# Kernel tuning notes

Measured on AMD Instinct MI355X. Metric: run time of the kernel, lower is better.

Reference implementation:

```python
import jax, jax.numpy as jnp
import numpy as np

D_MODEL = 1024
NHEAD = 16
HEAD_DIM = D_MODEL // NHEAD
MASK_FILLER = -1e20


def setup_inputs() -> dict:
    key = jax.random.key(0)
    ks = jax.random.split(key, 8)
    B, S = 2, 2048
    query = jax.random.normal(ks[0], (B, S, D_MODEL), dtype=jnp.float32)
    key_t = jax.random.normal(ks[1], (B, S, D_MODEL), dtype=jnp.float32)
    value = jax.random.normal(ks[2], (B, S, D_MODEL), dtype=jnp.float32)
    mask = jax.random.randint(ks[3], (B, S, S), 0, 2, dtype=jnp.int32)
    # nn.Linear(d_model, d_model, bias=False) weights, shape [out, in]
    scale = 1.0 / np.sqrt(D_MODEL)
    wq = jax.random.uniform(ks[4], (D_MODEL, D_MODEL), jnp.float32, -scale, scale)
    wk = jax.random.uniform(ks[5], (D_MODEL, D_MODEL), jnp.float32, -scale, scale)
    wv = jax.random.uniform(ks[6], (D_MODEL, D_MODEL), jnp.float32, -scale, scale)
    wo = jax.random.uniform(ks[7], (D_MODEL, D_MODEL), jnp.float32, -scale, scale)
    return {"query": query, "key": key_t, "value": value, "mask": mask,
            "wq": wq, "wk": wk, "wv": wv, "wo": wo}


def reference(query, key, value, mask, wq, wk, wv, wo):
    B = query.shape[0]
    # Projections: nn.Linear -> x @ W.T
    q = (query @ wq.T).reshape(B, -1, NHEAD, HEAD_DIM).transpose(0, 2, 1, 3)  # [B,H,Sq,Dh]
    k = (key @ wk.T).reshape(B, -1, NHEAD, HEAD_DIM).transpose(0, 2, 1, 3)    # [B,H,Sk,Dh]
    v = (value @ wv.T).reshape(B, -1, NHEAD, HEAD_DIM).transpose(0, 2, 1, 3)  # [B,H,Sk,Dh]
    scores = jnp.einsum('bhqd,bhkd->bhqk', q, k) / jnp.sqrt(jnp.float32(HEAD_DIM))
    scores = jnp.where(mask[:, None, :, :] == 0, MASK_FILLER, scores)
    attn = jax.nn.softmax(scores, axis=-1)  # dropout p=0.0 -> identity
    out = jnp.einsum('bhqk,bhkd->bhqd', attn, v)  # [B,H,Sq,Dh]
    out = out.transpose(0, 2, 1, 3).reshape(B, -1, D_MODEL)
    return out @ wo.T
```

## Files before the change

kernel.cpp:

```cpp
#include <hip/hip_runtime.h>
#include <stdint.h>

typedef __bf16 bf16x8 __attribute__((ext_vector_type(8)));
typedef float floatx4 __attribute__((ext_vector_type(4)));
typedef unsigned short ushort8v __attribute__((ext_vector_type(8)));
typedef unsigned int uint4v __attribute__((ext_vector_type(4)));
typedef unsigned int uint2v __attribute__((ext_vector_type(2)));
typedef unsigned short u16;
typedef unsigned long long u64;

#define GLOAD_LDS16(gp, lp)                                                       \
  __builtin_amdgcn_global_load_lds((__attribute__((address_space(1))) void*)(gp), \
                                   (__attribute__((address_space(3))) void*)(lp), \
                                   16, 0, 0)

__device__ __forceinline__ u16 f2bf(float f) {
  uint32_t u = __builtin_bit_cast(uint32_t, f);
  u = (u + 0x7FFFu + ((u >> 16) & 1u)) >> 16;
  return (u16)u;
}

__device__ __forceinline__ ushort8v load8(const void* base, size_t elemOff, int isf32) {
  if (isf32) {
    const uint32_t* p = (const uint32_t*)base + elemOff;
    uint4v a = *(const uint4v*)p;
    uint4v b = *(const uint4v*)(p + 4);
#pragma unroll
    for (int i = 0; i < 4; ++i) { a[i] += 0x8000u; b[i] += 0x8000u; }
    uint4v r;
    r[0] = __builtin_amdgcn_perm(a[1], a[0], 0x07060302);
    r[1] = __builtin_amdgcn_perm(a[3], a[2], 0x07060302);
    r[2] = __builtin_amdgcn_perm(b[1], b[0], 0x07060302);
    r[3] = __builtin_amdgcn_perm(b[3], b[2], 0x07060302);
    return __builtin_bit_cast(ushort8v, r);
  }
  return *(const ushort8v*)((const u16*)base + elemOff);
}

__global__ void detect_dtype(const u16* __restrict__ q, int* __restrict__ flag) {
  if (threadIdx.x == 0) *flag = 0;
  __syncthreads();
  int hit = 0;
  for (int i = threadIdx.x; i < 8192; i += 256) {
    u16 u = q[i];
    if (((u >> 7) & 0xFF) == 0xFF) hit = 1;
  }
  if (hit) atomicOr(flag, 1);
}

__global__ __launch_bounds__(256)
void prep(const void* X0, const void* X1, const void* X2,
          const void* W0, const void* W1, const void* W2, const void* W3,
          u16* __restrict__ Xb, u16* __restrict__ Wb,
          const int* __restrict__ mask, u64* __restrict__ mpk,
          const int* __restrict__ flagp)
{
  const int id = blockIdx.x;
  const int t  = threadIdx.x;
  if (id < 8192) {
    const int isf = *flagp;
    const int r2  = t >> 7;
    const int col = (t & 127) * 8;
    const void* src; u16* dst; int row;
    if (id < 6144) {
      const int s = id >> 11;
      src = (s == 0) ? X0 : (s == 1) ? X1 : X2;
      row = (id & 2047) * 2 + r2;
      dst = Xb + (size_t)s * 4096 * 1040 + (size_t)row * 1040 + col;
    } else {
      const int s = (id - 6144) >> 9;
      src = (s == 0) ? W0 : (s == 1) ? W1 : (s == 2) ? W2 : W3;
      row = ((id - 6144) & 511) * 2 + r2;
      dst = Wb + (size_t)s * 1024 * 1040 + (size_t)row * 1040 + col;
    }
    *(ushort8v*)dst = load8(src, (size_t)row * 1024 + col, isf);
  } else {
    const int g    = (id - 8192) * 4 + (t >> 6);
    const int lane = t & 63;
#pragma unroll
    for (int i = 0; i < 4; ++i) {
      const int wordId = g * 4 + i;
      const int row  = wordId >> 5;
      const int word = wordId & 31;
      const int m = mask[(size_t)row * 2048 + word * 64 + lane];
      u64 bits = __ballot(m != 0);
      if (lane == 0) mpk[(size_t)row * 32 + word] = bits;
    }
  }
}

__global__ void pack_mask(const int* __restrict__ mask, u64* __restrict__ mpk) {
  const int gw   = (blockIdx.x * 256 + threadIdx.x) >> 6;
  const int lane = threadIdx.x & 63;
  const int word = gw & 31;
  const int row  = gw >> 5;
  const int m = mask[(size_t)row * 2048 + word * 64 + lane];
  u64 bits = __ballot(m != 0);
  if (lane == 0) mpk[(size_t)row * 32 + word] = bits;
}

__global__ __launch_bounds__(256)
void cvt_w(const void* W0, const void* W1, const void* W2, const void* W3,
           u16* __restrict__ dst, const int* __restrict__ flagp) {
  const int isf = *flagp;
  const int z = blockIdx.y;
  const void* src = (z == 0) ? W0 : (z == 1) ? W1 : (z == 2) ? W2 : W3;
  const size_t off = ((size_t)blockIdx.x * 256 + threadIdx.x) * 8;
  *(ushort8v*)(dst + (size_t)z * 1024 * 1024 + off) = load8(src, off, isf);
}

__global__ __launch_bounds__(256, 3)
void gemm_qkv_b(const u16* __restrict__ Xb, const u16* __restrict__ Wb,
                u16* __restrict__ Qb, u16* __restrict__ Kb, u16* __restrict__ Vt)
{
  const int AS = 1040, WS = 1040, N = 1024, K = 1024;
  const int z = blockIdx.z;
  const u16* A = Xb + (size_t)z * 4096 * AS;
  const u16* W = Wb + (size_t)z * 1024 * WS;

  __shared__ __align__(16) u16 lA[2 * 128 * 32];
  __shared__ __align__(16) u16 lB[2 * 128 * 32];

  const int tid  = threadIdx.x;
  const int lane = tid & 63;
  const int quad = lane >> 4;
  const int l15  = lane & 15;
  const int w    = tid >> 6;
  const int wm   = w >> 1, wn = w & 1;
  const int tileM = blockIdx.x * 128;
  const int tileN = blockIdx.y * 128;

  floatx4 acc[4][4] = {};

  const int ldRow = tid >> 2;
  const int ldCol = (tid & 3) * 8;
  const u16* aG = A + (size_t)(tileM + ldRow) * AS + ldCol;
  const u16* bG = W + (size_t)(tileN + ldRow) * WS + ldCol;
  u16* lAp = lA + tid * 8;
  u16* lBp = lB + tid * 8;

  GLOAD_LDS16(aG, lAp);
  GLOAD_LDS16(aG + (size_t)64 * AS, lAp + 2048);
  GLOAD_LDS16(bG, lBp);
  GLOAD_LDS16(bG + (size_t)64 * WS, lBp + 2048);
  __syncthreads();

#pragma unroll 2
  for (int k0 = 0; k0 < K; k0 += 32) {
    const int cur = (k0 >> 5) & 1;
    const int nxo = 4096 * (cur ^ 1);
    if (k0 + 32 < K) {
      GLOAD_LDS16(aG + k0 + 32, lAp + nxo);
      GLOAD_LDS16(aG + (size_t)64 * AS + k0 + 32, lAp + nxo + 2048);
      GLOAD_LDS16(bG + k0 + 32, lBp + nxo);
      GLOAD_LDS16(bG + (size_t)64 * WS + k0 + 32, lBp + nxo + 2048);
    }
    const u16* cA = lA + 4096 * cur;
    const u16* cB = lB + 4096 * cur;
    bf16x8 af[4], bw[4];
#pragma unroll
    for (int i = 0; i < 4; ++i) {
      af[i] = *(const bf16x8*)&cA[(wm * 64 + i * 16 + l15) * 32 + quad * 8];
      bw[i] = *(const bf16x8*)&cB[(wn * 64 + i * 16 + l15) * 32 + quad * 8];
    }
#pragma unroll
    for (int i = 0; i < 4; ++i)
#pragma unroll
      for (int j = 0; j < 4; ++j)
        acc[i][j] = __builtin_amdgcn_mfma_f32_16x16x32_bf16(af[i], bw[j], acc[i][j], 0, 0, 0);
    __syncthreads();
  }

  if (z < 2) {
    u16* C = (z == 0) ? Qb : Kb;
    const float sc = (z == 0) ? 0.18033688011112042f : 1.0f;
#pragma unroll
    for (int i = 0; i < 4; ++i) {
      const int row0 = tileM + wm * 64 + i * 16 + quad * 4;
#pragma unroll
      for (int j = 0; j < 4; ++j) {
        const int col = tileN + wn * 64 + j * 16 + l15;
#pragma unroll
        for (int r = 0; r < 4; ++r)
          C[(size_t)(row0 + r) * N + col] = f2bf(acc[i][j][r] * sc);
      }
    }
  } else {
    const int half = w >> 1;
    u16* myT = (w & 1) ? lB : lA;
#pragma unroll
    for (int pass = 0; pass < 2; ++pass) {
      __syncthreads();
      if (half == pass) {
#pragma unroll
        for (int i = 0; i < 4; ++i)
#pragma unroll
          for (int j = 0; j < 4; ++j)
#pragma unroll
            for (int r = 0; r < 4; ++r) {
              const int lr = i * 16 + quad * 4 + r;
              const int lc = j * 16 + l15;
              myT[lr * 64 + (lc ^ (quad << 4))] = f2bf(acc[i][j][r]);
            }
      }
      __syncthreads();
      if (half == pass) {
        const int n    = lane;
        const int gcol = tileN + wn * 64 + n;
        const int hh = gcol >> 6, dd = gcol & 63;
        const int growBase = tileM + wm * 64;
        const int bb = growBase >> 11;
        const int s0 = growBase & 2047;
        u16* dst = Vt + (((size_t)bb * 16 + hh) * 64 + dd) * 2048 + s0;
#pragma unroll
        for (int m0 = 0; m0 < 64; m0 += 8) {
          ushort8v pk;
#pragma unroll
          for (int t = 0; t < 8; ++t) {
            const int m = m0 + t;
            pk[t] = myT[m * 64 + (n ^ ((m & 12) << 2))];
          }
          *(ushort8v*)(dst + m0) = pk;
        }
      }
    }
  }
}

__global__ __launch_bounds__(256)
void gemm_qkv_f(const void* X0, const void* X1, const void* X2,
                const u16* __restrict__ Wb,
                u16* __restrict__ Qb, u16* __restrict__ Kb, u16* __restrict__ Vt,
                const int* __restrict__ flagp)
{
  const int K = 1024, N = 1024;
  const int isf = *flagp;
  const int z = blockIdx.z;
  const void* A_ = (z == 0) ? X0 : (z == 1) ? X1 : X2;
  const u16* W = Wb + (size_t)z * 1024 * 1024;

  __shared__ __align__(16) u16 lA[128 * 32];
  __shared__ __align__(16) u16 lB[128 * 32];

  const int tid  = threadIdx.x;
  const int lane = tid & 63;
  const int quad = lane >> 4;
  const int l15  = lane & 15;
  const int w    = tid >> 6;
  const int wm   = w >> 1, wn = w & 1;
  const int tileM = blockIdx.x * 128;
  const int tileN = blockIdx.y * 128;

  floatx4 acc[4][4] = {};

  const int ldRow = tid >> 2;
  const int ldCol = (tid & 3) * 8;
  const size_t aOff = (size_t)(tileM + ldRow) * K + ldCol;
  const u16* bG = W + (size_t)(tileN + ldRow) * K + ldCol;
  u16* lAp = lA + tid * 8;
  u16* lBp = lB + tid * 8;

  ushort8v a0 = load8(A_, aOff, isf);
  ushort8v a1 = load8(A_, aOff + (size_t)64 * K, isf);
  ushort8v b0 = *(const ushort8v*)bG;
  ushort8v b1 = *(const ushort8v*)(bG + (size_t)64 * K);

  for (int k0 = 0; k0 < K; k0 += 32) {
    __syncthreads();
    *(ushort8v*)lAp          = a0;
    *(ushort8v*)(lAp + 2048) = a1;
    *(ushort8v*)lBp          = b0;
    *(ushort8v*)(lBp + 2048) = b1;
    __syncthreads();

    if (k0 + 32 < K) {
      a0 = load8(A_, aOff + k0 + 32, isf);
      a1 = load8(A_, aOff + (size_t)64 * K + k0 + 32, isf);
      b0 = *(const ushort8v*)(bG + k0 + 32);
      b1 = *(const ushort8v*)(bG + (size_t)64 * K + k0 + 32);
    }

    bf16x8 af[4], bw[4];
#pragma unroll
    for (int i = 0; i < 4; ++i) {
      af[i] = *(const bf16x8*)&lA[(wm * 64 + i * 16 + l15) * 32 + quad * 8];
      bw[i] = *(const bf16x8*)&lB[(wn * 64 + i * 16 + l15) * 32 + quad * 8];
    }
#pragma unroll
    for (int i = 0; i < 4; ++i)
#pragma unroll
      for (int j = 0; j < 4; ++j)
        acc[i][j] = __builtin_amdgcn_mfma_f32_16x16x32_bf16(af[i], bw[j], acc[i][j], 0, 0, 0);
  }

  if (z < 2) {
    u16* C = (z == 0) ? Qb : Kb;
    const float sc = (z == 0) ? 0.18033688011112042f : 1.0f;
#pragma unroll
    for (int i = 0; i < 4; ++i) {
      const int row0 = tileM + wm * 64 + i * 16 + quad * 4;
#pragma unroll
      for (int j = 0; j < 4; ++j) {
        const int col = tileN + wn * 64 + j * 16 + l15;
#pragma unroll
        for (int r = 0; r < 4; ++r)
          C[(size_t)(row0 + r) * N + col] = f2bf(acc[i][j][r] * sc);
      }
    }
  } else {
    const int half = w >> 1;
    u16* myT = (w & 1) ? lB : lA;
#pragma unroll
    for (int pass = 0; pass < 2; ++pass) {
      __syncthreads();
      if (half == pass) {
#pragma unroll
        for (int i = 0; i < 4; ++i)
#pragma unroll
          for (int j = 0; j < 4; ++j)
#pragma unroll
            for (int r = 0; r < 4; ++r) {
              const int lr = i * 16 + quad * 4 + r;
              const int lc = j * 16 + l15;
              myT[lr * 64 + (lc ^ (quad << 4))] = f2bf(acc[i][j][r]);
            }
      }
      __syncthreads();
      if (half == pass) {
        const int n    = lane;
        const int gcol = tileN + wn * 64 + n;
        const int hh = gcol >> 6, dd = gcol & 63;
        const int growBase = tileM + wm * 64;
        const int bb = growBase >> 11;
        const int s0 = growBase & 2047;
        u16* dst = Vt + (((size_t)bb * 16 + hh) * 64 + dd) * 2048 + s0;
#pragma unroll
        for (int m0 = 0; m0 < 64; m0 += 8) {
          ushort8v pk;
#pragma unroll
          for (int t = 0; t < 8; ++t) {
            const int m = m0 + t;
            pk[t] = myT[m * 64 + (n ^ ((m & 12) << 2))];
          }
          *(ushort8v*)(dst + m0) = pk;
        }
      }
    }
  }
}

__global__ __launch_bounds__(256)
void attn(const u16* Qb, const u16* __restrict__ Kb, const u16* __restrict__ Vt,
          const u64* __restrict__ mpk, u16* AO, int aoStr)
{
  __shared__ __align__(16) u16 lK[2][64 * 64];
  __shared__ __align__(16) u16 lV[64 * 64];
  __shared__ __align__(16) u16 lP[4][16 * 64];

  const int tid  = threadIdx.x;
  const int lane = tid & 63;
  const int quad = lane >> 4;
  const int l15  = lane & 15;
  const int w    = tid >> 6;

  const int bh = blockIdx.x;
  const int qt = blockIdx.y;
  const int b  = bh >> 4;
  const int h  = bh & 15;
  const size_t rowB   = (size_t)b * 2048;
  const size_t vtBase = ((size_t)bh * 64) * 2048;

  bf16x8 aq[2];
  {
    const u16* qp = Qb + (rowB + qt * 64 + w * 16 + l15) * 1024 + h * 64 + quad * 8;
    aq[0] = *(const bf16x8*)qp;
    aq[1] = *(const bf16x8*)(qp + 32);
  }

  const ushort8v one_u = {0x3F80, 0x3F80, 0x3F80, 0x3F80, 0x3F80, 0x3F80, 0x3F80, 0x3F80};
  const bf16x8 ones = __builtin_bit_cast(bf16x8, one_u);

  floatx4 o[4], l4;
#pragma unroll
  for (int nb = 0; nb < 4; ++nb) o[nb] = (floatx4){0.f, 0.f, 0.f, 0.f};
  l4 = (floatx4){0.f, 0.f, 0.f, 0.f};

  const u64* mrow = mpk + (rowB + qt * 64 + w * 16 + l15) * 32;
  u16* lPw = &lP[w][0];

  const int r1 = tid >> 3;
  const int cs = ((tid & 7) ^ (r1 & 7)) * 8;
  const u16* kSrc = Kb + (rowB + r1) * 1024 + h * 64 + cs;
  const u16* vSrc = Vt + vtBase + (size_t)r1 * 2048 + cs;

  GLOAD_LDS16(kSrc,                     &lK[0][tid * 8]);
  GLOAD_LDS16(kSrc + (size_t)32 * 1024, &lK[0][tid * 8 + 2048]);

#pragma unroll 2
  for (int kt = 0; kt < 32; ++kt) {
    const int cur = kt & 1;
    __syncthreads();

    {
      const u16* vS = vSrc + kt * 64;
      GLOAD_LDS16(vS,                     &lV[tid * 8]);
      GLOAD_LDS16(vS + (size_t)32 * 2048, &lV[tid * 8 + 2048]);
    }
    if (kt < 31) {
      const u16* kS = kSrc + (size_t)(kt + 1) * 64 * 1024;
      GLOAD_LDS16(kS,                     &lK[cur ^ 1][tid * 8]);
      GLOAD_LDS16(kS + (size_t)32 * 1024, &lK[cur ^ 1][tid * 8 + 2048]);
    }

    const u64 mw = mrow[kt];

#pragma unroll
    for (int nb = 0; nb < 4; ++nb) {
      const int row = nb * 16 + l15;
      const int swk = (row & 7) << 3;
      bf16x8 ak0 = *(const bf16x8*)&lK[cur][row * 64 + ((quad * 8) ^ swk)];
      bf16x8 ak1 = *(const bf16x8*)&lK[cur][row * 64 + ((quad * 8 + 32) ^ swk)];
      floatx4 sacc = {0.f, 0.f, 0.f, 0.f};
      sacc = __builtin_amdgcn_mfma_f32_16x16x32_bf16(ak0, aq[0], sacc, 0, 0, 0);
      sacc = __builtin_amdgcn_mfma_f32_16x16x32_bf16(ak1, aq[1], sacc, 0, 0, 0);
      const uint32_t nib = (uint32_t)(mw >> (nb * 16 + quad * 4)) & 0xFu;
      float p0 = (nib & 1u) ? __builtin_amdgcn_exp2f(sacc[0]) : 0.0f;
      float p1 = (nib & 2u) ? __builtin_amdgcn_exp2f(sacc[1]) : 0.0f;
      float p2 = (nib & 4u) ? __builtin_amdgcn_exp2f(sacc[2]) : 0.0f;
      float p3 = (nib & 8u) ? __builtin_amdgcn_exp2f(sacc[3]) : 0.0f;
      const uint32_t b0 = __builtin_bit_cast(uint32_t, p0) + 0x8000u;
      const uint32_t b1 = __builtin_bit_cast(uint32_t, p1) + 0x8000u;
      const uint32_t b2 = __builtin_bit_cast(uint32_t, p2) + 0x8000u;
      const uint32_t b3 = __builtin_bit_cast(uint32_t, p3) + 0x8000u;
      uint2v pk2;
      pk2[0] = __builtin_amdgcn_perm(b1, b0, 0x07060302);
      pk2[1] = __builtin_amdgcn_perm(b3, b2, 0x07060302);
      const int col = (nb * 16 + quad * 4) ^ ((l15 & 7) << 3);
      *(uint2v*)&lPw[l15 * 64 + col] = pk2;
    }
    __syncthreads();

#pragma unroll
    for (int ks = 0; ks < 2; ++ks) {
      bf16x8 ap = *(const bf16x8*)&lPw[l15 * 64 + ((ks * 32 + quad * 8) ^ ((l15 & 7) << 3))];
#pragma unroll
      for (int nb = 0; nb < 4; ++nb) {
        const int row = nb * 16 + l15;
        bf16x8 bv = *(const bf16x8*)&lV[row * 64 + ((ks * 32 + quad * 8) ^ ((row & 7) << 3))];
        o[nb] = __builtin_amdgcn_mfma_f32_16x16x32_bf16(ap, bv, o[nb], 0, 0, 0);
      }
      l4 = __builtin_amdgcn_mfma_f32_16x16x32_bf16(ap, ones, l4, 0, 0, 0);
    }
  }

#pragma unroll
  for (int r = 0; r < 4; ++r) {
    const float inv = 1.0f / l4[r];
    const size_t orow = (rowB + qt * 64 + w * 16 + quad * 4 + r) * aoStr + h * 64;
#pragma unroll
    for (int nb = 0; nb < 4; ++nb)
      AO[orow + nb * 16 + l15] = f2bf(o[nb][r] * inv);
  }
}

__global__ __launch_bounds__(256, 3)
void gemm_out(const u16* __restrict__ A, int aStr,
              const u16* __restrict__ W, int wStr, void* C_,
              const int* __restrict__ flagp)
{
  const int K = 1024, N = 1024;
  const int isf = *flagp;

  __shared__ __align__(16) u16 lA[2 * 64 * 32];
  __shared__ __align__(16) u16 lB[2 * 128 * 32];

  const int tid  = threadIdx.x;
  const int lane = tid & 63;
  const int quad = lane >> 4;
  const int l15  = lane & 15;
  const int w    = tid >> 6;
  const int tileM = blockIdx.x * 64;
  const int tileN = blockIdx.y * 128;

  floatx4 acc[4][2] = {};

  const int ldRow = tid >> 2;
  const int ldCol = (tid & 3) * 8;
  const u16* aG = A + (size_t)(tileM + ldRow) * aStr + ldCol;
  const u16* bG = W + (size_t)(tileN + ldRow) * wStr + ldCol;
  u16* lAp = lA + tid * 8;
  u16* lBp = lB + tid * 8;

  GLOAD_LDS16(aG, lAp);
  GLOAD_LDS16(bG, lBp);
  GLOAD_LDS16(bG + (size_t)64 * wStr, lBp + 2048);
  __syncthreads();

#pragma unroll 2
  for (int k0 = 0; k0 < K; k0 += 32) {
    const int cur = (k0 >> 5) & 1;
    const int nxA = 2048 * (cur ^ 1);
    const int nxB = 4096 * (cur ^ 1);
    if (k0 + 32 < K) {
      GLOAD_LDS16(aG + k0 + 32, lAp + nxA);
      GLOAD_LDS16(bG + k0 + 32, lBp + nxB);
      GLOAD_LDS16(bG + (size_t)64 * wStr + k0 + 32, lBp + nxB + 2048);
    }
    const u16* cA = lA + 2048 * cur;
    const u16* cB = lB + 4096 * cur;
    bf16x8 af[4], bw[2];
#pragma unroll
    for (int i = 0; i < 4; ++i)
      af[i] = *(const bf16x8*)&cA[(i * 16 + l15) * 32 + quad * 8];
#pragma unroll
    for (int j = 0; j < 2; ++j)
      bw[j] = *(const bf16x8*)&cB[(w * 32 + j * 16 + l15) * 32 + quad * 8];
#pragma unroll
    for (int i = 0; i < 4; ++i)
#pragma unroll
      for (int j = 0; j < 2; ++j)
        acc[i][j] = __builtin_amdgcn_mfma_f32_16x16x32_bf16(af[i], bw[j], acc[i][j], 0, 0, 0);
    __syncthreads();
  }

#pragma unroll
  for (int i = 0; i < 4; ++i) {
    const int row0 = tileM + i * 16 + quad * 4;
#pragma unroll
    for (int j = 0; j < 2; ++j) {
      const int col = tileN + w * 32 + j * 16 + l15;
#pragma unroll
      for (int r = 0; r < 4; ++r) {
        const size_t off = (size_t)(row0 + r) * N + col;
        if (isf) ((float*)C_)[off] = acc[i][j][r];
        else     ((u16*)C_)[off]   = f2bf(acc[i][j][r]);
      }
    }
  }
}

extern "C" void kernel_launch(void* const* d_in, const int* in_sizes, int n_in,
                              void* d_out, int out_size, void* d_ws, size_t ws_size,
                              hipStream_t stream)
{
  const int* mk = (const int*)d_in[3];

  int* flag = (int*)d_ws;
  u64* mpk  = (u64*)((char*)d_ws + 256);
  const size_t SZ = (size_t)4096 * 1024;
  u16* Qb = (u16*)((char*)d_ws + 256 + (size_t)1048576);
  u16* Kb = Qb + SZ;
  u16* Vt = Kb + SZ;
  u16* Wb = Vt + SZ;

  const size_t WB_PAD = (size_t)4 * 1024 * 1040;
  const size_t XB_PAD = (size_t)3 * 4096 * 1040;
  const size_t NEED = 256 + 1048576 + 3 * SZ * 2 + WB_PAD * 2 + XB_PAD * 2;

  detect_dtype<<<1, 256, 0, stream>>>((const u16*)d_in[0], flag);

  if (ws_size >= NEED) {
    u16* Xb = Wb + WB_PAD;
    prep<<<16384, 256, 0, stream>>>(d_in[0], d_in[1], d_in[2],
                                    d_in[4], d_in[5], d_in[6], d_in[7],
                                    Xb, Wb, mk, mpk, flag);
    gemm_qkv_b<<<dim3(32, 8, 3), 256, 0, stream>>>(Xb, Wb, Qb, Kb, Vt);
    u16* AOp = Xb;
    attn<<<dim3(32, 32), 256, 0, stream>>>(Qb, Kb, Vt, mpk, AOp, 1040);
    gemm_out<<<dim3(64, 8), 256, 0, stream>>>(AOp, 1040,
                                              Wb + (size_t)3 * 1024 * 1040, 1040,
                                              d_out, flag);
  } else {
    pack_mask<<<32768, 256, 0, stream>>>(mk, mpk);
    cvt_w<<<dim3(512, 4), 256, 0, stream>>>(d_in[4], d_in[5], d_in[6], d_in[7], Wb, flag);
    gemm_qkv_f<<<dim3(32, 8, 3), 256, 0, stream>>>(d_in[0], d_in[1], d_in[2],
                                                   Wb, Qb, Kb, Vt, flag);
    attn<<<dim3(32, 32), 256, 0, stream>>>(Qb, Kb, Vt, mpk, Qb, 1024);
    gemm_out<<<dim3(64, 8), 256, 0, stream>>>(Qb, 1024,
                                              Wb + (size_t)3 * 1024 * 1024, 1024,
                                              d_out, flag);
  }
}
```

Baseline: 274.5 us.

## Software-pipeline attention loop: overlap QK of next tile with PV of previous

Restructures the attention inner loop into a software pipeline. QK^T and softmax for tile kt now run in the same iteration as the PV product for tile kt-1, with V and P double-buffered in LDS. This removes one barrier per iteration and lets MFMA work from both phases interleave with the exp2 work. In exchange it doubles LDS use for V and P, which may lower occupancy. It also switches the bf16 packing from a manual round-and-perm to compiler __bf16 conversions.

Result: slower. 305.3 us (+11.2%).

```diff
diff --git a/kernel.cpp b/kernel.cpp
--- a/kernel.cpp
+++ b/kernel.cpp
@@ -2,6 +2,7 @@
 #include <stdint.h>
 
 typedef __bf16 bf16x8 __attribute__((ext_vector_type(8)));
+typedef __bf16 bf16x4 __attribute__((ext_vector_type(4)));
 typedef float floatx4 __attribute__((ext_vector_type(4)));
 typedef unsigned short ushort8v __attribute__((ext_vector_type(8)));
 typedef unsigned int uint4v __attribute__((ext_vector_type(4)));
@@ -349,13 +350,64 @@
   }
 }
 
+#define MFMA_BF16 __builtin_amdgcn_mfma_f32_16x16x32_bf16
+
+#define QK_PHASE(KBUF, sacc)                                                    \
+  {                                                                             \
+    _Pragma("unroll")                                                           \
+    for (int nb = 0; nb < 4; ++nb) {                                            \
+      const int row = nb * 16 + l15;                                            \
+      const int swk = (row & 7) << 3;                                           \
+      bf16x8 ak0 = *(const bf16x8*)&(KBUF)[row * 64 + ((quad * 8) ^ swk)];      \
+      bf16x8 ak1 = *(const bf16x8*)&(KBUF)[row * 64 + ((quad * 8 + 32) ^ swk)]; \
+      floatx4 s = {0.f, 0.f, 0.f, 0.f};                                         \
+      s = MFMA_BF16(ak0, aq[0], s, 0, 0, 0);                                    \
+      s = MFMA_BF16(ak1, aq[1], s, 0, 0, 0);                                    \
+      sacc[nb] = s;                                                             \
+    }                                                                           \
+  }
+
+#define PV_PHASE(PBUF, VBUF)                                                    \
+  {                                                                             \
+    _Pragma("unroll")                                                           \
+    for (int ks = 0; ks < 2; ++ks) {                                            \
+      bf16x8 ap = *(const bf16x8*)&(PBUF)[l15 * 64 +                            \
+                    ((ks * 32 + quad * 8) ^ ((l15 & 7) << 3))];                 \
+      _Pragma("unroll")                                                         \
+      for (int nb = 0; nb < 4; ++nb) {                                          \
+        const int row = nb * 16 + l15;                                          \
+        bf16x8 bv = *(const bf16x8*)&(VBUF)[row * 64 +                          \
+                      ((ks * 32 + quad * 8) ^ ((row & 7) << 3))];               \
+        o[nb] = MFMA_BF16(ap, bv, o[nb], 0, 0, 0);                              \
+      }                                                                         \
+      l4 = MFMA_BF16(ap, ones, l4, 0, 0, 0);                                    \
+    }                                                                           \
+  }
+
+#define SM_PHASE(sacc, mw, PDST)                                                \
+  {                                                                             \
+    _Pragma("unroll")                                                           \
+    for (int nb = 0; nb < 4; ++nb) {                                            \
+      const uint32_t nib = (uint32_t)((mw) >> (nb * 16 + quad * 4)) & 0xFu;     \
+      const float p0 = (nib & 1u) ? __builtin_amdgcn_exp2f(sacc[nb][0]) : 0.0f; \
+      const float p1 = (nib & 2u) ? __builtin_amdgcn_exp2f(sacc[nb][1]) : 0.0f; \
+      const float p2 = (nib & 4u) ? __builtin_amdgcn_exp2f(sacc[nb][2]) : 0.0f; \
+      const float p3 = (nib & 8u) ? __builtin_amdgcn_exp2f(sacc[nb][3]) : 0.0f; \
+      bf16x4 pk4;                                                               \
+      pk4[0] = (__bf16)p0; pk4[1] = (__bf16)p1;                                 \
+      pk4[2] = (__bf16)p2; pk4[3] = (__bf16)p3;                                 \
+      const int col = (nb * 16 + quad * 4) ^ ((l15 & 7) << 3);                  \
+      *(bf16x4*)&(PDST)[l15 * 64 + col] = pk4;                                  \
+    }                                                                           \
+  }
+
 __global__ __launch_bounds__(256)
 void attn(const u16* Qb, const u16* __restrict__ Kb, const u16* __restrict__ Vt,
           const u64* __restrict__ mpk, u16* AO, int aoStr)
 {
   __shared__ __align__(16) u16 lK[2][64 * 64];
-  __shared__ __align__(16) u16 lV[64 * 64];
-  __shared__ __align__(16) u16 lP[4][16 * 64];
+  __shared__ __align__(16) u16 lV[2][64 * 64];
+  __shared__ __align__(16) u16 lP[2][4][16 * 64];
 
   const int tid  = threadIdx.x;
   const int lane = tid & 63;
@@ -386,7 +438,6 @@
   l4 = (floatx4){0.f, 0.f, 0.f, 0.f};
 
   const u64* mrow = mpk + (rowB + qt * 64 + w * 16 + l15) * 32;
-  u16* lPw = &lP[w][0];
 
   const int r1 = tid >> 3;
   const int cs = ((tid & 7) ^ (r1 & 7)) * 8;
@@ -395,63 +446,42 @@
 
   GLOAD_LDS16(kSrc,                     &lK[0][tid * 8]);
   GLOAD_LDS16(kSrc + (size_t)32 * 1024, &lK[0][tid * 8 + 2048]);
+  __syncthreads();
+  GLOAD_LDS16(kSrc + (size_t)64 * 1024, &lK[1][tid * 8]);
+  GLOAD_LDS16(kSrc + (size_t)96 * 1024, &lK[1][tid * 8 + 2048]);
+  GLOAD_LDS16(vSrc,                     &lV[0][tid * 8]);
+  GLOAD_LDS16(vSrc + (size_t)32 * 2048, &lV[0][tid * 8 + 2048]);
+  {
+    floatx4 sacc[4];
+    QK_PHASE(lK[0], sacc);
+    const u64 mw = mrow[0];
+    SM_PHASE(sacc, mw, &lP[0][w][0]);
+  }
 
 #pragma unroll 2
-  for (int kt = 0; kt < 32; ++kt) {
-    const int cur = kt & 1;
+  for (int kt = 1; kt < 32; ++kt) {
+    const int cur = kt & 1, prv = cur ^ 1;
     __syncthreads();
-
+    if (kt < 31) {
+      const u16* kS = kSrc + (size_t)(kt + 1) * 64 * 1024;
+      GLOAD_LDS16(kS,                     &lK[prv][tid * 8]);
+      GLOAD_LDS16(kS + (size_t)32 * 1024, &lK[prv][tid * 8 + 2048]);
+    }
     {
       const u16* vS = vSrc + kt * 64;
-      GLOAD_LDS16(vS,                     &lV[tid * 8]);
-      GLOAD_LDS16(vS + (size_t)32 * 2048, &lV[tid * 8 + 2048]);
-    }
-    if (kt < 31) {
-      const u16* kS = kSrc + (size_t)(kt + 1) * 64 * 1024;
-      GLOAD_LDS16(kS,                     &lK[cur ^ 1][tid * 8]);
-      GLOAD_LDS16(kS + (size_t)32 * 1024, &lK[cur ^ 1][tid * 8 + 2048]);
-    }
-
+      GLOAD_LDS16(vS,                     &lV[cur][tid * 8]);
+      GLOAD_LDS16(vS + (size_t)32 * 2048, &lV[cur][tid * 8 + 2048]);
+    }
+
+    floatx4 sacc[4];
+    QK_PHASE(lK[cur], sacc);
+    PV_PHASE(&lP[prv][w][0], lV[prv]);
     const u64 mw = mrow[kt];
-
-#pragma unroll
-    for (int nb = 0; nb < 4; ++nb) {
-      const int row = nb * 16 + l15;
-      const int swk = (row & 7) << 3;
-      bf16x8 ak0 = *(const bf16x8*)&lK[cur][row * 64 + ((quad * 8) ^ swk)];
-      bf16x8 ak1 = *(const bf16x8*)&lK[cur][row * 64 + ((quad * 8 + 32) ^ swk)];
-      floatx4 sacc = {0.f, 0.f, 0.f, 0.f};
-      sacc = __builtin_amdgcn_mfma_f32_16x16x32_bf16(ak0, aq[0], sacc, 0, 0, 0);
-      sacc = __builtin_amdgcn_mfma_f32_16x16x32_bf16(ak1, aq[1], sacc, 0, 0, 0);
-      const uint32_t nib = (uint32_t)(mw >> (nb * 16 + quad * 4)) & 0xFu;
-      float p0 = (nib & 1u) ? __builtin_amdgcn_exp2f(sacc[0]) : 0.0f;
-      float p1 = (nib & 2u) ? __builtin_amdgcn_exp2f(sacc[1]) : 0.0f;
-      float p2 = (nib & 4u) ? __builtin_amdgcn_exp2f(sacc[2]) : 0.0f;
-      float p3 = (nib & 8u) ? __builtin_amdgcn_exp2f(sacc[3]) : 0.0f;
-      const uint32_t b0 = __builtin_bit_cast(uint32_t, p0) + 0x8000u;
-      const uint32_t b1 = __builtin_bit_cast(uint32_t, p1) + 0x8000u;
-      const uint32_t b2 = __builtin_bit_cast(uint32_t, p2) + 0x8000u;
-      const uint32_t b3 = __builtin_bit_cast(uint32_t, p3) + 0x8000u;
-      uint2v pk2;
-      pk2[0] = __builtin_amdgcn_perm(b1, b0, 0x07060302);
-      pk2[1] = __builtin_amdgcn_perm(b3, b2, 0x07060302);
-      const int col = (nb * 16 + quad * 4) ^ ((l15 & 7) << 3);
-      *(uint2v*)&lPw[l15 * 64 + col] = pk2;
-    }
-    __syncthreads();
-
-#pragma unroll
-    for (int ks = 0; ks < 2; ++ks) {
-      bf16x8 ap = *(const bf16x8*)&lPw[l15 * 64 + ((ks * 32 + quad * 8) ^ ((l15 & 7) << 3))];
-#pragma unroll
-      for (int nb = 0; nb < 4; ++nb) {
-        const int row = nb * 16 + l15;
-        bf16x8 bv = *(const bf16x8*)&lV[row * 64 + ((ks * 32 + quad * 8) ^ ((row & 7) << 3))];
-        o[nb] = __builtin_amdgcn_mfma_f32_16x16x32_bf16(ap, bv, o[nb], 0, 0, 0);
-      }
-      l4 = __builtin_amdgcn_mfma_f32_16x16x32_bf16(ap, ones, l4, 0, 0, 0);
-    }
-  }
+    SM_PHASE(sacc, mw, &lP[cur][w][0]);
+  }
+
+  __syncthreads();
+  PV_PHASE(&lP[1][w][0], lV[1]);
 
 #pragma unroll
   for (int r = 0; r < 4; ++r) {
```

## Process 32 query rows per wave in attention to double K/V tile reuse

Applied to the files above, without the earlier changes.

Each wave in the attention kernel now computes scores and PV products for two 16-row query groups instead of one, so every block covers 128 query rows and the grid's query dimension is halved. Each K and V tile loaded into LDS is therefore reused across twice as many queries, which cuts global-to-LDS traffic and barrier overhead per unit of work. The P buffer in LDS doubles in size and the register count for accumulators grows. The manual bf16 rounding of the probabilities is replaced by a native __bf16 conversion. The risk is fewer resident blocks, 512 in total, and lower occupancy to hide latency.

After: 272.1 us. Within noise of the previous version (-0.9%).

```diff
diff --git a/kernel.cpp b/kernel.cpp
--- a/kernel.cpp
+++ b/kernel.cpp
@@ -2,10 +2,10 @@
 #include <stdint.h>
 
 typedef __bf16 bf16x8 __attribute__((ext_vector_type(8)));
+typedef __bf16 bf16x4 __attribute__((ext_vector_type(4)));
 typedef float floatx4 __attribute__((ext_vector_type(4)));
 typedef unsigned short ushort8v __attribute__((ext_vector_type(8)));
 typedef unsigned int uint4v __attribute__((ext_vector_type(4)));
-typedef unsigned int uint2v __attribute__((ext_vector_type(2)));
 typedef unsigned short u16;
 typedef unsigned long long u64;
 
@@ -355,7 +355,7 @@
 {
   __shared__ __align__(16) u16 lK[2][64 * 64];
   __shared__ __align__(16) u16 lV[64 * 64];
-  __shared__ __align__(16) u16 lP[4][16 * 64];
+  __shared__ __align__(16) u16 lP[4][32 * 64];
 
   const int tid  = threadIdx.x;
   const int lane = tid & 63;
@@ -369,23 +369,30 @@
   const int h  = bh & 15;
   const size_t rowB   = (size_t)b * 2048;
   const size_t vtBase = ((size_t)bh * 64) * 2048;
-
-  bf16x8 aq[2];
-  {
-    const u16* qp = Qb + (rowB + qt * 64 + w * 16 + l15) * 1024 + h * 64 + quad * 8;
-    aq[0] = *(const bf16x8*)qp;
-    aq[1] = *(const bf16x8*)(qp + 32);
+  const int qbase = qt * 128 + w * 32;
+
+  bf16x8 aq[2][2];
+#pragma unroll
+  for (int g = 0; g < 2; ++g) {
+    const u16* qp = Qb + (rowB + qbase + g * 16 + l15) * 1024 + h * 64 + quad * 8;
+    aq[g][0] = *(const bf16x8*)qp;
+    aq[g][1] = *(const bf16x8*)(qp + 32);
   }
 
   const ushort8v one_u = {0x3F80, 0x3F80, 0x3F80, 0x3F80, 0x3F80, 0x3F80, 0x3F80, 0x3F80};
   const bf16x8 ones = __builtin_bit_cast(bf16x8, one_u);
 
-  floatx4 o[4], l4;
-#pragma unroll
-  for (int nb = 0; nb < 4; ++nb) o[nb] = (floatx4){0.f, 0.f, 0.f, 0.f};
-  l4 = (floatx4){0.f, 0.f, 0.f, 0.f};
-
-  const u64* mrow = mpk + (rowB + qt * 64 + w * 16 + l15) * 32;
+  floatx4 o[2][4];
+  floatx4 l4[2];
+#pragma unroll
+  for (int g = 0; g < 2; ++g) {
+    l4[g] = (floatx4){0.f, 0.f, 0.f, 0.f};
+#pragma unroll
+    for (int nb = 0; nb < 4; ++nb) o[g][nb] = (floatx4){0.f, 0.f, 0.f, 0.f};
+  }
+
+  const u64* mrow0 = mpk + (rowB + qbase + l15) * 32;
+  const u64* mrow1 = mpk + (rowB + qbase + 16 + l15) * 32;
   u16* lPw = &lP[w][0];
 
   const int r1 = tid >> 3;
@@ -412,7 +419,8 @@
       GLOAD_LDS16(kS + (size_t)32 * 1024, &lK[cur ^ 1][tid * 8 + 2048]);
     }
 
-    const u64 mw = mrow[kt];
+    const u64 mw0 = mrow0[kt];
+    const u64 mw1 = mrow1[kt];
 
 #pragma unroll
     for (int nb = 0; nb < 4; ++nb) {
@@ -420,47 +428,61 @@
       const int swk = (row & 7) << 3;
       bf16x8 ak0 = *(const bf16x8*)&lK[cur][row * 64 + ((quad * 8) ^ swk)];
       bf16x8 ak1 = *(const bf16x8*)&lK[cur][row * 64 + ((quad * 8 + 32) ^ swk)];
-      floatx4 sacc = {0.f, 0.f, 0.f, 0.f};
-      sacc = __builtin_amdgcn_mfma_f32_16x16x32_bf16(ak0, aq[0], sacc, 0, 0, 0);
-      sacc = __builtin_amdgcn_mfma_f32_16x16x32_bf16(ak1, aq[1], sacc, 0, 0, 0);
-      const uint32_t nib = (uint32_t)(mw >> (nb * 16 + quad * 4)) & 0xFu;
-      float p0 = (nib & 1u) ? __builtin_amdgcn_exp2f(sacc[0]) : 0.0f;
-      float p1 = (nib & 2u) ? __builtin_amdgcn_exp2f(sacc[1]) : 0.0f;
-      float p2 = (nib & 4u) ? __builtin_amdgcn_exp2f(sacc[2]) : 0.0f;
-      float p3 = (nib & 8u) ? __builtin_amdgcn_exp2f(sacc[3]) : 0.0f;
-      const uint32_t b0 = __builtin_bit_cast(uint32_t, p0) + 0x8000u;
-      const uint32_t b1 = __builtin_bit_cast(uint32_t, p1) + 0x8000u;
-      const uint32_t b2 = __builtin_bit_cast(uint32_t, p2) + 0x8000u;
-      const uint32_t b3 = __builtin_bit_cast(uint32_t, p3) + 0x8000u;
-      uint2v pk2;
-      pk2[0] = __builtin_amdgcn_perm(b1, b0, 0x07060302);
-      pk2[1] = __builtin_amdgcn_perm(b3, b2, 0x07060302);
-      const int col = (nb * 16 + quad * 4) ^ ((l15 & 7) << 3);
-      *(uint2v*)&lPw[l15 * 64 + col] = pk2;
+      floatx4 s0 = {0.f, 0.f, 0.f, 0.f};
+      floatx4 s1 = {0.f, 0.f, 0.f, 0.f};
+      s0 = __builtin_amdgcn_mfma_f32_16x16x32_bf16(ak0, aq[0][0], s0, 0, 0, 0);
+      s1 = __builtin_amdgcn_mfma_f32_16x16x32_bf16(ak0, aq[1][0], s1, 0, 0, 0);
+      s0 = __builtin_amdgcn_mfma_f32_16x16x32_bf16(ak1, aq[0][1], s0, 0, 0, 0);
+      s1 = __builtin_amdgcn_mfma_f32_16x16x32_bf16(ak1, aq[1][1], s1, 0, 0, 0);
+      const int kb = nb * 16 + quad * 4;
+      const uint32_t nib0 = (uint32_t)(mw0 >> kb) & 0xFu;
+      const uint32_t nib1 = (uint32_t)(mw1 >> kb) & 0xFu;
+      const float a0 = (nib0 & 1u) ? __builtin_amdgcn_exp2f(s0[0]) : 0.0f;
+      const float a1 = (nib0 & 2u) ? __builtin_amdgcn_exp2f(s0[1]) : 0.0f;
+      const float a2 = (nib0 & 4u) ? __builtin_amdgcn_exp2f(s0[2]) : 0.0f;
+      const float a3 = (nib0 & 8u) ? __builtin_amdgcn_exp2f(s0[3]) : 0.0f;
+      const float c0 = (nib1 & 1u) ? __builtin_amdgcn_exp2f(s1[0]) : 0.0f;
+      const float c1 = (nib1 & 2u) ? __builtin_amdgcn_exp2f(s1[1]) : 0.0f;
+      const float c2 = (nib1 & 4u) ? __builtin_amdgcn_exp2f(s1[2]) : 0.0f;
+      const float c3 = (nib1 & 8u) ? __builtin_amdgcn_exp2f(s1[3]) : 0.0f;
+      bf16x4 p0, p1;
+      p0[0] = (__bf16)a0; p0[1] = (__bf16)a1;
+      p0[2] = (__bf16)a2; p0[3] = (__bf16)a3;
+      p1[0] = (__bf16)c0; p1[1] = (__bf16)c1;
+      p1[2] = (__bf16)c2; p1[3] = (__bf16)c3;
+      const int col = kb ^ ((l15 & 7) << 3);
+      *(bf16x4*)&lPw[l15 * 64 + col]        = p0;
+      *(bf16x4*)&lPw[(16 + l15) * 64 + col] = p1;
     }
     __syncthreads();
 
 #pragma unroll
     for (int ks = 0; ks < 2; ++ks) {
-      bf16x8 ap = *(const bf16x8*)&lPw[l15 * 64 + ((ks * 32 + quad * 8) ^ ((l15 & 7) << 3))];
+      const int pc = (ks * 32 + quad * 8) ^ ((l15 & 7) << 3);
+      bf16x8 ap0 = *(const bf16x8*)&lPw[l15 * 64 + pc];
+      bf16x8 ap1 = *(const bf16x8*)&lPw[(16 + l15) * 64 + pc];
 #pragma unroll
       for (int nb = 0; nb < 4; ++nb) {
         const int row = nb * 16 + l15;
         bf16x8 bv = *(const bf16x8*)&lV[row * 64 + ((ks * 32 + quad * 8) ^ ((row & 7) << 3))];
-        o[nb] = __builtin_amdgcn_mfma_f32_16x16x32_bf16(ap, bv, o[nb], 0, 0, 0);
-      }
-      l4 = __builtin_amdgcn_mfma_f32_16x16x32_bf16(ap, ones, l4, 0, 0, 0);
-    }
-  }
-
-#pragma unroll
-  for (int r = 0; r < 4; ++r) {
-    const float inv = 1.0f / l4[r];
-    const size_t orow = (rowB + qt * 64 + w * 16 + quad * 4 + r) * aoStr + h * 64;
-#pragma unroll
-    for (int nb = 0; nb < 4; ++nb)
-      AO[orow + nb * 16 + l15] = f2bf(o[nb][r] * inv);
-  }
+        o[0][nb] = __builtin_amdgcn_mfma_f32_16x16x32_bf16(ap0, bv, o[0][nb], 0, 0, 0);
+        o[1][nb] = __builtin_amdgcn_mfma_f32_16x16x32_bf16(ap1, bv, o[1][nb], 0, 0, 0);
+      }
+      l4[0] = __builtin_amdgcn_mfma_f32_16x16x32_bf16(ap0, ones, l4[0], 0, 0, 0);
+      l4[1] = __builtin_amdgcn_mfma_f32_16x16x32_bf16(ap1, ones, l4[1], 0, 0, 0);
+    }
+  }
+
+#pragma unroll
+  for (int g = 0; g < 2; ++g)
+#pragma unroll
+    for (int r = 0; r < 4; ++r) {
+      const float inv = 1.0f / l4[g][r];
+      const size_t orow = (rowB + qbase + g * 16 + quad * 4 + r) * aoStr + h * 64;
+#pragma unroll
+      for (int nb = 0; nb < 4; ++nb)
+        AO[orow + nb * 16 + l15] = f2bf(o[g][nb][r] * inv);
+    }
 }
 
 __global__ __launch_bounds__(256, 3)
@@ -566,7 +588,7 @@
                                     Xb, Wb, mk, mpk, flag);
     gemm_qkv_b<<<dim3(32, 8, 3), 256, 0, stream>>>(Xb, Wb, Qb, Kb, Vt);
     u16* AOp = Xb;
-    attn<<<dim3(32, 32), 256, 0, stream>>>(Qb, Kb, Vt, mpk, AOp, 1040);
+    attn<<<dim3(32, 16), 256, 0, stream>>>(Qb, Kb, Vt, mpk, AOp, 1040);
     gemm_out<<<dim3(64, 8), 256, 0, stream>>>(AOp, 1040,
                                               Wb + (size_t)3 * 1024 * 1040, 1040,
                                               d_out, flag);
@@ -575,7 +597,7 @@
     cvt_w<<<dim3(512, 4), 256, 0, stream>>>(d_in[4], d_in[5], d_in[6], d_in[7], Wb, flag);
     gemm_qkv_f<<<dim3(32, 8, 3), 256, 0, stream>>>(d_in[0], d_in[1], d_in[2],
                                                    Wb, Qb, Kb, Vt, flag);
-    attn<<<dim3(32, 32), 256, 0, stream>>>(Qb, Kb, Vt, mpk, Qb, 1024);
+    attn<<<dim3(32, 16), 256, 0, stream>>>(Qb, Kb, Vt, mpk, Qb, 1024);
     gemm_out<<<dim3(64, 8), 256, 0, stream>>>(Qb, 1024,
                                               Wb + (size_t)3 * 1024 * 1024, 1024,
                                               d_out, flag);
```
